# Kernel tuning notes

Hardware: AMD Instinct MI355X
Metric: run time of the kernel (lower is better)

## Reference

```python
import jax, jax.numpy as jnp
import numpy as np

INPUT_SIZE = 2
HIDDEN = 128
OUTPUT = 2
FUTURE = 50


def setup_inputs() -> dict:
    key = jax.random.key(0)
    ks = jax.random.split(key, 7)
    B, T = 4096, 512
    s = 1.0 / np.sqrt(HIDDEN)
    x = jax.random.normal(ks[0], (B, T, INPUT_SIZE), dtype=jnp.float32)
    W_ih = jax.random.uniform(ks[1], (4 * HIDDEN, INPUT_SIZE), minval=-s, maxval=s, dtype=jnp.float32)
    W_hh = jax.random.uniform(ks[2], (4 * HIDDEN, HIDDEN), minval=-s, maxval=s, dtype=jnp.float32)
    b_ih = jax.random.uniform(ks[3], (4 * HIDDEN,), minval=-s, maxval=s, dtype=jnp.float32)
    b_hh = jax.random.uniform(ks[4], (4 * HIDDEN,), minval=-s, maxval=s, dtype=jnp.float32)
    fc_w = jax.random.uniform(ks[5], (OUTPUT, HIDDEN), minval=-s, maxval=s, dtype=jnp.float32)
    fc_b = jax.random.uniform(ks[6], (OUTPUT,), minval=-s, maxval=s, dtype=jnp.float32)
    return {"x": x, "W_ih": W_ih, "W_hh": W_hh, "b_ih": b_ih, "b_hh": b_hh, "fc_w": fc_w, "fc_b": fc_b}


def reference(x, W_ih, W_hh, b_ih, b_hh, fc_w, fc_b):
    B = x.shape[0]

    def cell(h, c, xt):
        # gates: [B, 4H], PyTorch LSTMCell order i, f, g, o
        gates = xt @ W_ih.T + b_ih + h @ W_hh.T + b_hh
        i, f, g, o = jnp.split(gates, 4, axis=-1)
        c_new = jax.nn.sigmoid(f) * c + jax.nn.sigmoid(i) * jnp.tanh(g)
        h_new = jax.nn.sigmoid(o) * jnp.tanh(c_new)
        return h_new, c_new

    h0 = jnp.zeros((B, HIDDEN), dtype=x.dtype)
    c0 = jnp.zeros((B, HIDDEN), dtype=x.dtype)

    def encode_step(carry, xt):
        h, c = carry
        h, c = cell(h, c, xt)
        return (h, c), None

    (h, c), _ = jax.lax.scan(encode_step, (h0, c0), jnp.swapaxes(x, 0, 1))

    def forecast_step(carry, _):
        h, c = carry
        y = h @ fc_w.T + fc_b  # [B, OUTPUT]
        h, c = cell(h, c, y)
        return (h, c), y

    (_, _), ys = jax.lax.scan(forecast_step, (h, c), None, length=FUTURE)
    # ys: [FUTURE, B, OUTPUT] -> torch.cat(outputs, dim=1) -> [B, FUTURE*OUTPUT]
    return jnp.swapaxes(ys, 0, 1).reshape(B, FUTURE * OUTPUT)
```

## Files before the change

### kernel.cpp

```cpp
#include <hip/hip_runtime.h>

#define HIDDEN 128
#define TSTEPS 512
#define NFUT 50
#define BR 16
#define THREADS 512
#define HPITCH 136

typedef __bf16 bf16x8 __attribute__((ext_vector_type(8)));
typedef float floatx4 __attribute__((ext_vector_type(4)));

union B8 { int4 i; bf16x8 v; };

#if defined(__has_builtin)
#  if __has_builtin(__builtin_amdgcn_exp2f)
#    define EXP2F(x) __builtin_amdgcn_exp2f(x)
#  else
#    define EXP2F(x) exp2f(x)
#  endif
#  if __has_builtin(__builtin_amdgcn_rcpf)
#    define RCPF(x) __builtin_amdgcn_rcpf(x)
#  else
#    define RCPF(x) (1.0f / (x))
#  endif
#else
#  define EXP2F(x) exp2f(x)
#  define RCPF(x) (1.0f / (x))
#endif

#define L2E  1.4426950408889634f
#define L2E2 2.8853900817779268f

__global__ __launch_bounds__(THREADS, 2)
void lstm_forecast_kernel(const float* __restrict__ x,
                          const float* __restrict__ W_ih,
                          const float* __restrict__ W_hh,
                          const float* __restrict__ b_ih,
                          const float* __restrict__ b_hh,
                          const float* __restrict__ fc_w,
                          const float* __restrict__ fc_b,
                          float* __restrict__ out) {
    __shared__ __align__(16) uint2  xa[TSTEPS * BR];
    __shared__ __align__(16) __bf16 h_lds[2][BR * HPITCH];
    __shared__ __align__(16) float  fcw_lds[2][HIDDEN];

    const int tid  = threadIdx.x;
    const int wave = tid >> 6;
    const int lane = tid & 63;
    const int quad = lane >> 4;
    const int l15  = lane & 15;
    const int rb   = blockIdx.x * BR;

    if (tid < 256) fcw_lds[tid >> 7][tid & 127] = fc_w[tid];

    {
        const int row = tid & 15;
        for (int tb = tid >> 4; tb < TSTEPS; tb += THREADS >> 4) {
            float2 xv = *(const float2*)&x[(size_t)(rb + row) * (2 * TSTEPS) + tb * 2];
            __bf16 x0h = (__bf16)xv.x, x1h = (__bf16)xv.y;
            __bf16 x0r = (__bf16)(xv.x - (float)x0h);
            __bf16 x1r = (__bf16)(xv.y - (float)x1h);
            uint2 d;
            d.x = (unsigned)__builtin_bit_cast(unsigned short, x0h) |
                  ((unsigned)__builtin_bit_cast(unsigned short, x1h) << 16);
            d.y = (unsigned)__builtin_bit_cast(unsigned short, x0r) |
                  ((unsigned)__builtin_bit_cast(unsigned short, x1r) << 16);
            xa[tb * BR + row] = d;
        }
    }
    for (int i = tid; i < BR * HPITCH; i += THREADS) h_lds[0][i] = (__bf16)0.0f;

    bf16x8 bfrag[4][4];
    B8 bfx[4];
    float wih0[4], wih1[4], bsum[4], gs[4];
    const int u = wave * 16 + l15;
    const float fcb0 = fc_b[0], fcb1 = fc_b[1];
#pragma unroll
    for (int g = 0; g < 4; ++g) {
        gs[g] = (g == 2) ? -L2E2 : -L2E;
        const int cg = g * HIDDEN + u;
        wih0[g] = W_ih[cg * 2 + 0];
        wih1[g] = W_ih[cg * 2 + 1];
        bsum[g] = b_ih[cg] + b_hh[cg];
#pragma unroll
        for (int ks = 0; ks < 4; ++ks) {
            const float* wp = W_hh + (size_t)cg * HIDDEN + ks * 32 + quad * 8;
            bf16x8 bb;
#pragma unroll
            for (int j = 0; j < 8; ++j) bb[j] = (__bf16)(gs[g] * wp[j]);
            bfrag[g][ks] = bb;
        }
        B8 t; t.i = make_int4(0, 0, 0, 0);
        if (quad == 0) {
            const float w0s = gs[g] * wih0[g], w1s = gs[g] * wih1[g], bss = gs[g] * bsum[g];
            __bf16 w0h = (__bf16)w0s, w1h = (__bf16)w1s;
            __bf16 w0l = (__bf16)(w0s - (float)w0h);
            __bf16 w1l = (__bf16)(w1s - (float)w1h);
            __bf16 bh  = (__bf16)bss;
            __bf16 bl  = (__bf16)(bss - (float)bh);
            bf16x8 bv = {w0h, w1h, bh, bl, w0h, w1h, w0l, w1l};
            t.v = bv;
        }
        bfx[g] = t;
    }

    const unsigned ones2 = 0x3F803F80u;

    float cst[4] = {0.f, 0.f, 0.f, 0.f};

    auto ew = [&](floatx4 a0, floatx4 a1, floatx4 a2, floatx4 a3, __bf16* hd) {
#pragma unroll
        for (int reg = 0; reg < 4; ++reg) {
            const float ea = EXP2F(a0[reg]);
            const float eb = EXP2F(a2[reg]);
            const float ec = EXP2F(a1[reg]);
            const float A1 = 1.f + ea, B1 = 1.f + eb, C1 = 1.f + ec;
            const float P  = A1 * B1;
            const float R  = RCPF(P * C1);
            const float sfv = P * R;
            const float igv = (1.f - eb) * C1 * R;
            const float cn  = fmaf(sfv, cst[reg], igv);
            cst[reg] = cn;
            const float arg = fminf(-L2E2 * cn, 80.f);
            const float ed  = EXP2F(arg);
            const float eo  = EXP2F(a3[reg]);
            const float R2  = RCPF((1.f + ed) * (1.f + eo));
            const float hn  = (1.f - ed) * R2;
            hd[(quad * 4 + reg) * HPITCH + u] = (__bf16)hn;
        }
    };

    auto cellE = [&](const __bf16* hs, __bf16* hd, int t) {
        const uint2 xd = xa[t * BR + l15];
        B8 xf; xf.i = make_int4((int)xd.x, (int)ones2, (int)xd.y, (int)xd.x);
        bf16x8 af[4];
#pragma unroll
        for (int ks = 0; ks < 4; ++ks)
            af[ks] = *(const bf16x8*)&hs[l15 * HPITCH + ks * 32 + quad * 8];
        const floatx4 z = {0.f, 0.f, 0.f, 0.f};
        floatx4 acc[4];
#pragma unroll
        for (int g = 0; g < 4; ++g)
            acc[g] = __builtin_amdgcn_mfma_f32_16x16x32_bf16(xf.v, bfx[g].v, z, 0, 0, 0);
#pragma unroll
        for (int ks = 0; ks < 4; ++ks)
#pragma unroll
            for (int g = 0; g < 4; ++g)
                acc[g] = __builtin_amdgcn_mfma_f32_16x16x32_bf16(af[ks], bfrag[g][ks], acc[g], 0, 0, 0);
        ew(acc[0], acc[1], acc[2], acc[3], hd);
        __syncthreads();
    };

    __syncthreads();

    for (int t = 0; t < TSTEPS; t += 2) {
        cellE(h_lds[0], h_lds[1], t);
        cellE(h_lds[1], h_lds[0], t + 1);
    }

    float bs2[4];
#pragma unroll
    for (int g = 0; g < 4; ++g) {
        bs2[g] = gs[g] * (bsum[g] + wih0[g] * fcb0 + wih1[g] * fcb1);
#pragma unroll
        for (int ks = 0; ks < 4; ++ks) {
            const int k0 = ks * 32 + quad * 8;
            bf16x8 bb = bfrag[g][ks];
#pragma unroll
            for (int j = 0; j < 8; ++j) {
                const float wv = (float)bb[j] + gs[g] * (wih0[g] * fcw_lds[0][k0 + j]
                                                      + wih1[g] * fcw_lds[1][k0 + j]);
                bb[j] = (__bf16)wv;
            }
            bfrag[g][ks] = bb;
        }
    }

    auto cellF = [&](const __bf16* hs, __bf16* hd) {
        bf16x8 af[4];
#pragma unroll
        for (int ks = 0; ks < 4; ++ks)
            af[ks] = *(const bf16x8*)&hs[l15 * HPITCH + ks * 32 + quad * 8];
        floatx4 acc[4];
#pragma unroll
        for (int g = 0; g < 4; ++g)
            acc[g] = (floatx4){bs2[g], bs2[g], bs2[g], bs2[g]};
#pragma unroll
        for (int ks = 0; ks < 4; ++ks)
#pragma unroll
            for (int g = 0; g < 4; ++g)
                acc[g] = __builtin_amdgcn_mfma_f32_16x16x32_bf16(af[ks], bfrag[g][ks], acc[g], 0, 0, 0);
        ew(acc[0], acc[1], acc[2], acc[3], hd);
        __syncthreads();
    };

    auto emitY = [&](const __bf16* hs, int f) {
        if (wave == 0) {
            const int r = lane & 15, seg = lane >> 4;
            const __bf16* hp = &hs[r * HPITCH + seg * 32];
            float p0 = 0.f, p1 = 0.f;
#pragma unroll
            for (int js = 0; js < 4; ++js) {
                bf16x8 hv = *(const bf16x8*)&hp[js * 8];
                const float4* f0 = (const float4*)&fcw_lds[0][seg * 32 + js * 8];
                const float4* f1 = (const float4*)&fcw_lds[1][seg * 32 + js * 8];
                float4 a0 = f0[0], b0 = f0[1], a1 = f1[0], b1 = f1[1];
                p0 += (float)hv[0]*a0.x + (float)hv[1]*a0.y + (float)hv[2]*a0.z + (float)hv[3]*a0.w
                    + (float)hv[4]*b0.x + (float)hv[5]*b0.y + (float)hv[6]*b0.z + (float)hv[7]*b0.w;
                p1 += (float)hv[0]*a1.x + (float)hv[1]*a1.y + (float)hv[2]*a1.z + (float)hv[3]*a1.w
                    + (float)hv[4]*b1.x + (float)hv[5]*b1.y + (float)hv[6]*b1.z + (float)hv[7]*b1.w;
            }
            p0 += __shfl_xor(p0, 16); p0 += __shfl_xor(p0, 32);
            p1 += __shfl_xor(p1, 16); p1 += __shfl_xor(p1, 32);
            if (seg == 0) {
                float* op = &out[(size_t)(rb + r) * (2 * NFUT) + f * 2];
                op[0] = p0 + fcb0;
                op[1] = p1 + fcb1;
            }
        }
    };

    for (int f = 0; f < NFUT; f += 2) {
        emitY(h_lds[0], f);
        cellF(h_lds[0], h_lds[1]);
        emitY(h_lds[1], f + 1);
        cellF(h_lds[1], h_lds[0]);
    }
}

extern "C" void kernel_launch(void* const* d_in, const int* in_sizes, int n_in,
                              void* d_out, int out_size, void* d_ws, size_t ws_size,
                              hipStream_t stream) {
    const float* x    = (const float*)d_in[0];
    const float* W_ih = (const float*)d_in[1];
    const float* W_hh = (const float*)d_in[2];
    const float* b_ih = (const float*)d_in[3];
    const float* b_hh = (const float*)d_in[4];
    const float* fc_w = (const float*)d_in[5];
    const float* fc_b = (const float*)d_in[6];
    float* out = (float*)d_out;

    const int B = in_sizes[0] / (TSTEPS * 2);
    const int grid = B / BR;
    lstm_forecast_kernel<<<grid, THREADS, 0, stream>>>(x, W_ih, W_hh, b_ih, b_hh, fc_w, fc_b, out);
}
```

Baseline: 514.0 us.

## Prefetch next-step input MFMA before barrier and batch reciprocals in gate math

Moves the input-projection MFMA for the next timestep to before the per-step barrier, so it overlaps with barrier wait instead of sitting on the recurrent critical path. The xa buffer is padded by one zero step to allow this lookahead. The forecast phase uses the same pattern, with a bias-only MFMA. The elementwise gate math now shares one reciprocal across four rows using Montgomery-style batched inversion, cutting RCP instructions at the cost of more multiplies. The tanh clamp is lowered to keep the batched product from overflowing.

```diff
diff --git a/kernel.cpp b/kernel.cpp
--- a/kernel.cpp
+++ b/kernel.cpp
@@ -40,7 +40,7 @@
                           const float* __restrict__ fc_w,
                           const float* __restrict__ fc_b,
                           float* __restrict__ out) {
-    __shared__ __align__(16) uint2  xa[TSTEPS * BR];
+    __shared__ __align__(16) uint2  xa[(TSTEPS + 1) * BR];
     __shared__ __align__(16) __bf16 h_lds[2][BR * HPITCH];
     __shared__ __align__(16) float  fcw_lds[2][HIDDEN];
 
@@ -55,8 +55,10 @@
 
     {
         const int row = tid & 15;
-        for (int tb = tid >> 4; tb < TSTEPS; tb += THREADS >> 4) {
-            float2 xv = *(const float2*)&x[(size_t)(rb + row) * (2 * TSTEPS) + tb * 2];
+        for (int tb = tid >> 4; tb < TSTEPS + 1; tb += THREADS >> 4) {
+            float2 xv = make_float2(0.f, 0.f);
+            if (tb < TSTEPS)
+                xv = *(const float2*)&x[(size_t)(rb + row) * (2 * TSTEPS) + tb * 2];
             __bf16 x0h = (__bf16)xv.x, x1h = (__bf16)xv.y;
             __bf16 x0r = (__bf16)(xv.x - (float)x0h);
             __bf16 x1r = (__bf16)(xv.y - (float)x1h);
@@ -109,59 +111,99 @@
     float cst[4] = {0.f, 0.f, 0.f, 0.f};
 
     auto ew = [&](floatx4 a0, floatx4 a1, floatx4 a2, floatx4 a3, __bf16* hd) {
-#pragma unroll
-        for (int reg = 0; reg < 4; ++reg) {
-            const float ea = EXP2F(a0[reg]);
-            const float eb = EXP2F(a2[reg]);
-            const float ec = EXP2F(a1[reg]);
-            const float A1 = 1.f + ea, B1 = 1.f + eb, C1 = 1.f + ec;
-            const float P  = A1 * B1;
-            const float R  = RCPF(P * C1);
-            const float sfv = P * R;
-            const float igv = (1.f - eb) * C1 * R;
-            const float cn  = fmaf(sfv, cst[reg], igv);
-            cst[reg] = cn;
-            const float arg = fminf(-L2E2 * cn, 80.f);
-            const float ed  = EXP2F(arg);
-            const float eo  = EXP2F(a3[reg]);
-            const float R2  = RCPF((1.f + ed) * (1.f + eo));
-            const float hn  = (1.f - ed) * R2;
-            hd[(quad * 4 + reg) * HPITCH + u] = (__bf16)hn;
+        float ea[4], eb[4], ec[4], A1[4], B1[4], C1[4], D[4];
+#pragma unroll
+        for (int r = 0; r < 4; ++r) {
+            ea[r] = EXP2F(a0[r]);
+            eb[r] = EXP2F(a2[r]);
+            ec[r] = EXP2F(a1[r]);
+            A1[r] = 1.f + ea[r];
+            B1[r] = 1.f + eb[r];
+            C1[r] = 1.f + ec[r];
+            D[r]  = A1[r] * B1[r] * C1[r];
+        }
+        const float p2 = D[0] * D[1], p3 = p2 * D[2], p4 = p3 * D[3];
+        const float I  = RCPF(p4);
+        const float R3 = I * p3;
+        const float I3 = I * D[3];
+        const float Rr2 = I3 * p2;
+        const float I2 = I3 * D[2];
+        const float R1 = I2 * D[0];
+        const float R0 = I2 * D[1];
+        const float Rr[4] = {R0, R1, Rr2, R3};
+        float cnv[4];
+#pragma unroll
+        for (int r = 0; r < 4; ++r) {
+            const float sfv = (A1[r] * B1[r]) * Rr[r];
+            const float igv = (1.f - eb[r]) * (C1[r] * Rr[r]);
+            cnv[r] = fmaf(sfv, cst[r], igv);
+            cst[r] = cnv[r];
+        }
+        float ed[4], eo[4], E[4];
+#pragma unroll
+        for (int r = 0; r < 4; ++r) {
+            const float arg = fminf(-L2E2 * cnv[r], 29.f);
+            ed[r] = EXP2F(arg);
+            eo[r] = EXP2F(a3[r]);
+            E[r]  = (1.f + ed[r]) * (1.f + eo[r]);
+        }
+        const float q2 = E[0] * E[1], q3 = q2 * E[2], q4 = q3 * E[3];
+        const float J  = RCPF(q4);
+        const float S3 = J * q3;
+        const float J3 = J * E[3];
+        const float S2 = J3 * q2;
+        const float J2 = J3 * E[2];
+        const float S1 = J2 * E[0];
+        const float S0 = J2 * E[1];
+        const float S[4] = {S0, S1, S2, S3};
+#pragma unroll
+        for (int r = 0; r < 4; ++r) {
+            const float hn = (1.f - ed[r]) * S[r];
+            hd[(quad * 4 + r) * HPITCH + u] = (__bf16)hn;
         }
     };
 
-    auto cellE = [&](const __bf16* hs, __bf16* hd, int t) {
-        const uint2 xd = xa[t * BR + l15];
+    __syncthreads();
+
+    floatx4 acc[4];
+    const floatx4 z = {0.f, 0.f, 0.f, 0.f};
+    {
+        const uint2 xd = xa[0 * BR + l15];
         B8 xf; xf.i = make_int4((int)xd.x, (int)ones2, (int)xd.y, (int)xd.x);
+#pragma unroll
+        for (int g = 0; g < 4; ++g)
+            acc[g] = __builtin_amdgcn_mfma_f32_16x16x32_bf16(xf.v, bfx[g].v, z, 0, 0, 0);
+    }
+
+    auto cellE = [&](const __bf16* hs, __bf16* hd, int tn) {
         bf16x8 af[4];
 #pragma unroll
         for (int ks = 0; ks < 4; ++ks)
             af[ks] = *(const bf16x8*)&hs[l15 * HPITCH + ks * 32 + quad * 8];
-        const floatx4 z = {0.f, 0.f, 0.f, 0.f};
-        floatx4 acc[4];
-#pragma unroll
-        for (int g = 0; g < 4; ++g)
-            acc[g] = __builtin_amdgcn_mfma_f32_16x16x32_bf16(xf.v, bfx[g].v, z, 0, 0, 0);
 #pragma unroll
         for (int ks = 0; ks < 4; ++ks)
 #pragma unroll
             for (int g = 0; g < 4; ++g)
                 acc[g] = __builtin_amdgcn_mfma_f32_16x16x32_bf16(af[ks], bfrag[g][ks], acc[g], 0, 0, 0);
         ew(acc[0], acc[1], acc[2], acc[3], hd);
+        {
+            const uint2 xd = xa[tn * BR + l15];
+            B8 xf; xf.i = make_int4((int)xd.x, (int)ones2, (int)xd.y, (int)xd.x);
+#pragma unroll
+            for (int g = 0; g < 4; ++g)
+                acc[g] = __builtin_amdgcn_mfma_f32_16x16x32_bf16(xf.v, bfx[g].v, z, 0, 0, 0);
+        }
         __syncthreads();
     };
 
-    __syncthreads();
-
     for (int t = 0; t < TSTEPS; t += 2) {
-        cellE(h_lds[0], h_lds[1], t);
-        cellE(h_lds[1], h_lds[0], t + 1);
-    }
-
-    float bs2[4];
+        cellE(h_lds[0], h_lds[1], t + 1);
+        cellE(h_lds[1], h_lds[0], t + 2);
+    }
+
 #pragma unroll
     for (int g = 0; g < 4; ++g) {
-        bs2[g] = gs[g] * (bsum[g] + wih0[g] * fcb0 + wih1[g] * fcb1);
+        const float bs2 = gs[g] * (bsum[g] + wih0[g] * fcb0 + wih1[g] * fcb1);
 #pragma unroll
         for (int ks = 0; ks < 4; ++ks) {
             const int k0 = ks * 32 + quad * 8;
@@ -174,23 +216,36 @@
             }
             bfrag[g][ks] = bb;
         }
-    }
+        B8 t; t.i = make_int4(0, 0, 0, 0);
+        if (quad == 0) {
+            __bf16 bh = (__bf16)bs2;
+            __bf16 bl = (__bf16)(bs2 - (float)bh);
+            bf16x8 bv = {(__bf16)0.f, (__bf16)0.f, bh, bl,
+                         (__bf16)0.f, (__bf16)0.f, (__bf16)0.f, (__bf16)0.f};
+            t.v = bv;
+        }
+        bfx[g] = t;
+    }
+    B8 xfF; xfF.i = make_int4(0, (int)ones2, 0, 0);
+
+#pragma unroll
+    for (int g = 0; g < 4; ++g)
+        acc[g] = __builtin_amdgcn_mfma_f32_16x16x32_bf16(xfF.v, bfx[g].v, z, 0, 0, 0);
 
     auto cellF = [&](const __bf16* hs, __bf16* hd) {
         bf16x8 af[4];
 #pragma unroll
         for (int ks = 0; ks < 4; ++ks)
             af[ks] = *(const bf16x8*)&hs[l15 * HPITCH + ks * 32 + quad * 8];
-        floatx4 acc[4];
-#pragma unroll
-        for (int g = 0; g < 4; ++g)
-            acc[g] = (floatx4){bs2[g], bs2[g], bs2[g], bs2[g]};
 #pragma unroll
         for (int ks = 0; ks < 4; ++ks)
 #pragma unroll
             for (int g = 0; g < 4; ++g)
                 acc[g] = __builtin_amdgcn_mfma_f32_16x16x32_bf16(af[ks], bfrag[g][ks], acc[g], 0, 0, 0);
         ew(acc[0], acc[1], acc[2], acc[3], hd);
+#pragma unroll
+        for (int g = 0; g < 4; ++g)
+            acc[g] = __builtin_amdgcn_mfma_f32_16x16x32_bf16(xfF.v, bfx[g].v, z, 0, 0, 0);
         __syncthreads();
     };
 
```

After: 538.1 us. 4.7% more time.
